# Optimization experiments

Measured on AMD Instinct MI355X. Metric: run time of the kernel, lower is better.

Reference implementation:

```python
import jax, jax.numpy as jnp
import numpy as np

# Production-scale dims (see shape_source)
T, H, W, C = 2, 384, 384, 128
HEADS, WIN = 4, 8
HD = C // HEADS            # head_dim = 32
SCALE = HD ** -0.5
N = WIN * WIN              # tokens per window = 64
DN = ('NCHW', 'OIHW', 'NCHW')


def setup_inputs() -> dict:
    key = jax.random.key(0)
    ks = jax.random.split(key, 16)
    p = lambda k, shp: jax.random.normal(k, shp, jnp.float32) * 0.02
    inp = {
        'vid': jax.random.normal(ks[0], (T, H, W, C), jnp.float32),
        'rpb_table': p(ks[1], ((2 * WIN - 1) * (2 * WIN - 1), HEADS)),
    }
    i = 2
    for nm in ('q', 'k', 'v'):  # SepConv2d: depthwise 3x3 + ReLU + pointwise 1x1
        inp[nm + '_dw'] = p(ks[i], (C, 1, 3, 3)); i += 1
        inp[nm + '_dwb'] = p(ks[i], (C,)); i += 1
        inp[nm + '_pw'] = p(ks[i], (C, C, 1, 1)); i += 1
        inp[nm + '_pwb'] = p(ks[i], (C,)); i += 1
    inp['proj_w'] = p(ks[14], (C, C))
    inp['proj_b'] = p(ks[15], (C,))
    return inp


def _sepconv(x, dw, dwb, pw, pwb):
    # x: [T, C, H, W]; Uformer SepConv2d = depthwise 3x3 -> ReLU -> pointwise 1x1
    y = jax.lax.conv_general_dilated(x, dw, (1, 1), 'SAME',
                                     feature_group_count=C, dimension_numbers=DN)
    y = jax.nn.relu(y + dwb[None, :, None, None])
    y = jax.lax.conv_general_dilated(y, pw, (1, 1), 'SAME', dimension_numbers=DN)
    return y + pwb[None, :, None, None]


def _to_windows(x):
    # [T, C, H, W] -> [T*nWh*nWw, heads, N, hd]
    x = x.reshape(T, HEADS, HD, H // WIN, WIN, W // WIN, WIN)
    x = x.transpose(0, 3, 5, 1, 4, 6, 2)
    return x.reshape(-1, HEADS, N, HD)


def _rel_bias(rpb_table):
    # Swin-style relative position index for an 8x8 window
    r = jnp.arange(WIN)
    coords = jnp.stack(jnp.meshgrid(r, r, indexing='ij')).reshape(2, -1)  # [2, N]
    rel = coords[:, :, None] - coords[:, None, :]                          # [2, N, N]
    idx = (rel[0] + WIN - 1) * (2 * WIN - 1) + (rel[1] + WIN - 1)          # [N, N]
    return rpb_table[idx].transpose(2, 0, 1)                               # [heads, N, N]


def reference(vid, rpb_table,
              q_dw, q_dwb, q_pw, q_pwb,
              k_dw, k_dwb, k_pw, k_pwb,
              v_dw, v_dwb, v_pw, v_pwb,
              proj_w, proj_b):
    x = vid.transpose(0, 3, 1, 2)                      # t h w c -> t c h w
    q = _sepconv(x, q_dw, q_dwb, q_pw, q_pwb) * SCALE  # q scaled as in forward
    k = _sepconv(x, k_dw, k_dwb, k_pw, k_pwb)
    v = _sepconv(x, v_dw, v_dwb, v_pw, v_pwb)
    qw, kw, vw = _to_windows(q), _to_windows(k), _to_windows(v)
    # rel-pos-biased softmax attention within each 8x8 window (ws==8 branch)
    attn = jnp.einsum('whnd,whmd->whnm', qw, kw) + _rel_bias(rpb_table)[None]
    attn = jax.nn.softmax(attn, axis=-1)
    out = jnp.einsum('whnm,whmd->whnd', attn, vw)      # weighted patch sum (ps=1)
    out = out.transpose(0, 2, 1, 3).reshape(-1, N, C)  # merge heads -> [nW, N, C]
    out = out @ proj_w.T + proj_b                      # nn.Linear(dim, dim)
    # windows back to video; iFoldz with ps=1, stride0=1 => zvid==1 (identity norm)
    Hn, Wn = H // WIN, W // WIN
    out = out.reshape(T, Hn, Wn, WIN, WIN, C).transpose(0, 1, 3, 2, 4, 5)
    return out.reshape(T, H, W, C)
```

## Files before the change

kernel.cpp:

```cpp
#include <hip/hip_runtime.h>
#include <hip/hip_fp16.h>
#include <stdint.h>

#define T_ 2
#define H_ 384
#define W_ 384
#define C_ 128
#define HN_ 48
#define WN_ 48
#define NWIN_ (T_*HN_*WN_)
#define SCALE_ 0.17677669529663687f

typedef float f32x4 __attribute__((ext_vector_type(4)));
typedef _Float16 f16x8 __attribute__((ext_vector_type(8)));

#define WS_WFRAG 0
#define WS_BIASX 131072
#define WS_DWF   196608
#define WS_DWB   205824

#define TMP_OFF 0
#define KB_OFF  16384
#define VB_OFF  32768
#define WL_OFF  49152
#define SMEM_SZ 81920

#define GLOBAL_AS __attribute__((address_space(1)))
#define LDS_AS    __attribute__((address_space(3)))

__device__ __forceinline__ void g2l16(const void* g, void* l){
  __builtin_amdgcn_global_load_lds((const GLOBAL_AS unsigned int*)g,
                                   (LDS_AS unsigned int*)l, 16, 0, 0);
}

__device__ __forceinline__ unsigned int pkh(float a, float b){
  union{__half2 h; unsigned int u;} c;
  c.h = __float22half2_rn(make_float2(a, b));
  return c.u;
}
__device__ __forceinline__ unsigned short f2h(float f){
  union{__half h; unsigned short u;} c; c.h = __float2half_rn(f); return c.u;
}
__device__ __forceinline__ __half2 u2h(unsigned int u){
  union{unsigned int u; __half2 h;} c; c.u = u; return c.h;
}
__device__ __forceinline__ unsigned int relu2u(__half2 v){
  union{__half2 h; unsigned int u;} c; c.h = v;
  const unsigned int m = ((c.u >> 15) & 0x00010001u) * 0xFFFFu;
  return c.u & ~m;
}
__device__ __forceinline__ int swz256(int row, int b){ return row*256 + (b ^ ((row & 15) << 4)); }
__device__ __forceinline__ int swz128(int row, int b){ return row*128 + (b ^ ((row & 7) << 4)); }

__device__ __forceinline__ f16x8 xpose_frag(uint2 a, uint2 b, int l0b, int l1b, int hi){
  union{ f16x8 v; unsigned int u[4]; } r;
  const unsigned x0 = __builtin_amdgcn_ds_bpermute(l0b, (int)a.x);
  const unsigned y0 = __builtin_amdgcn_ds_bpermute(l0b, (int)b.x);
  const unsigned x1 = __builtin_amdgcn_ds_bpermute(l0b, (int)a.y);
  const unsigned y1 = __builtin_amdgcn_ds_bpermute(l0b, (int)b.y);
  const unsigned x2 = __builtin_amdgcn_ds_bpermute(l1b, (int)a.x);
  const unsigned y2 = __builtin_amdgcn_ds_bpermute(l1b, (int)b.x);
  const unsigned x3 = __builtin_amdgcn_ds_bpermute(l1b, (int)a.y);
  const unsigned y3 = __builtin_amdgcn_ds_bpermute(l1b, (int)b.y);
  r.u[0] = hi ? y0 : x0; r.u[1] = hi ? y1 : x1;
  r.u[2] = hi ? y2 : x2; r.u[3] = hi ? y3 : x3;
  return r.v;
}

__global__ __launch_bounds__(256)
void prep_kernel(const float* __restrict__ qpw, const float* __restrict__ kpw,
                 const float* __restrict__ vpw, const float* __restrict__ pjw,
                 const float* __restrict__ rpb,
                 const float* __restrict__ qdw, const float* __restrict__ kdw,
                 const float* __restrict__ vdw,
                 const float* __restrict__ qdwb, const float* __restrict__ kdwb,
                 const float* __restrict__ vdwb,
                 ushort* __restrict__ wfrag, float* __restrict__ biasx,
                 unsigned int* __restrict__ dwf, unsigned int* __restrict__ dwb2)
{
  const int idx = blockIdx.x*256 + threadIdx.x;
  if (idx < 8192) {
    const int mat = idx >> 11, rem = idx & 2047;
    const int nt8 = rem >> 8, ks = (rem >> 6) & 3, lane = rem & 63;
    const int c16 = lane & 15, g = lane >> 4;
    const float* Ws[4] = {qpw, kpw, vpw, pjw};
    const float* src = Ws[mat] + (nt8*16 + c16)*128 + ks*32 + g*8;
    ushort* dst = wfrag + idx*8;
    #pragma unroll
    for (int e = 0; e < 8; ++e) dst[e] = f2h(src[e]);
  } else if (idx < 24576) {
    const int i2 = idx - 8192;
    const int he = i2 >> 12;
    const int m2 = (i2 >> 10) & 3;
    const int n  = (i2 >> 4) & 63;
    const int gr = i2 & 15;
    const int m  = m2*16 + gr;
    const int ny = n >> 3, nx = n & 7, my = m >> 3, mx = m & 7;
    biasx[i2] = rpb[((ny - my + 7)*15 + (nx - mx + 7))*4 + he];
  } else if (idx < 24576 + 2304) {
    const int i2 = idx - 24576;
    const int p = i2 / 768, rem = i2 % 768, cp = rem / 12, j = rem % 12;
    const float* dws[3] = {qdw, kdw, vdw};
    unsigned int v = 0;
    if (j < 9) v = pkh(dws[p][(2*cp)*9 + j], dws[p][(2*cp+1)*9 + j]);
    dwf[(p*64 + cp)*12 + j] = v;
  } else if (idx < 24576 + 2304 + 192) {
    const int i2 = idx - 24576 - 2304;
    const int p = i2 >> 6, cp = i2 & 63;
    const float* dbs[3] = {qdwb, kdwb, vdwb};
    dwb2[p*64 + cp] = pkh(dbs[p][2*cp], dbs[p][2*cp+1]);
  }
}

__global__ __launch_bounds__(512, 8)
void winattn_v4(const float* __restrict__ vid,
                const float* __restrict__ qpwb, const float* __restrict__ kpwb,
                const float* __restrict__ vpwb, const float* __restrict__ pjb,
                const ushort* __restrict__ wfrag, const float* __restrict__ biasx,
                const unsigned int* __restrict__ dwf, const unsigned int* __restrict__ dwb2,
                float* __restrict__ out)
{
  __shared__ __attribute__((aligned(16))) char smem[SMEM_SZ];
  char* tmpb = smem + TMP_OFF;
  char* kb   = smem + KB_OFF;
  char* vb   = smem + VB_OFF;
  char* wl   = smem + WL_OFF;

  const int tid  = threadIdx.x;
  const int w    = tid >> 6;
  const int lane = tid & 63;
  const int g    = lane >> 4;
  const int c16  = lane & 15;
  const int hi   = (lane >= 32);
  const int l0b  = (((g & 1) << 5) + c16) << 2;
  const int l1b  = l0b + 64;

  auto stage_w = [&](int m){
    const char* gsrc = reinterpret_cast<const char*>(wfrag) + m*32768;
    #pragma unroll
    for (int i2 = 0; i2 < 4; ++i2){
      const int off = (i2*512 + tid)*16;
      g2l16(gsrc + off, wl + off);
    }
  };

  const int wid = (blockIdx.x & 7) * (NWIN_ / 8) + (blockIdx.x >> 3);
  const int t  = wid / (HN_*WN_);
  const int hw = wid % (HN_*WN_);
  const int hn = hw / WN_, wn = hw % WN_;
  const int h0 = hn*8, w0 = wn*8;

  const int mt  = w & 3;
  const int ntb = (w >> 2) * 4;
  const int n0  = mt*16 + g*4;
  const int he = w >> 1, half = w & 1;
  const int y = w;

  stage_w(1);

  __half2 hx[3][10];
  #pragma unroll
  for (int dy = 0; dy < 3; ++dy){
    const int hh = h0 + y - 1 + dy;
    const bool rv = (unsigned)hh < (unsigned)H_;
    #pragma unroll
    for (int xc = 0; xc < 10; ++xc){
      const int ww = w0 - 1 + xc;
      float2 l = make_float2(0.f, 0.f);
      if (rv && (unsigned)ww < (unsigned)W_)
        l = *reinterpret_cast<const float2*>(&vid[(((long)t*H_ + hh)*W_ + ww)*C_ + 2*lane]);
      hx[dy][xc] = __float22half2_rn(l);
    }
  }

  auto dw_pass = [&](int p){
    const uint4* dq = reinterpret_cast<const uint4*>(dwf + (p*64 + lane)*12);
    const uint4 wA = dq[0], wB = dq[1], wC = dq[2];
    const __half2 w9[9] = { u2h(wA.x), u2h(wA.y), u2h(wA.z), u2h(wA.w),
                            u2h(wB.x), u2h(wB.y), u2h(wB.z), u2h(wB.w), u2h(wC.x) };
    const __half2 b2 = u2h(dwb2[p*64 + lane]);
    __half2 acc[8];
    #pragma unroll
    for (int px = 0; px < 8; ++px) acc[px] = b2;
    #pragma unroll
    for (int dy = 0; dy < 3; ++dy)
      #pragma unroll
      for (int dx = 0; dx < 3; ++dx){
        const __half2 w2 = w9[dy*3+dx];
        #pragma unroll
        for (int px = 0; px < 8; ++px)
          acc[px] = __hfma2(hx[dy][px+dx], w2, acc[px]);
      }
    #pragma unroll
    for (int px = 0; px < 8; ++px)
      *reinterpret_cast<unsigned int*>(tmpb + swz256(y*8+px, 4*lane)) = relu2u(acc[px]);
  };

  dw_pass(1);
  __syncthreads();
  {
    #pragma unroll
    for (int nh = 0; nh < 2; ++nh){
      f32x4 a2[2] = {{0.f,0.f,0.f,0.f},{0.f,0.f,0.f,0.f}};
      #pragma unroll
      for (int ks = 0; ks < 4; ++ks){
        const f16x8 af = *reinterpret_cast<const f16x8*>(tmpb + swz256(mt*16+c16, ks*64 + g*16));
        #pragma unroll
        for (int j = 0; j < 2; ++j){
          const f16x8 bf = *reinterpret_cast<const f16x8*>(wl + (((ntb+nh*2+j)*4 + ks)*64 + lane)*16);
          a2[j] = __builtin_amdgcn_mfma_f32_16x16x32_f16(af, bf, a2[j], 0, 0, 0);
        }
      }
      #pragma unroll
      for (int j = 0; j < 2; ++j){
        const int co = (ntb+nh*2+j)*16 + c16;
        const float bias = kpwb[co];
        const unsigned int u01 = pkh(a2[j][0]+bias, a2[j][1]+bias);
        const unsigned int u23 = pkh(a2[j][2]+bias, a2[j][3]+bias);
        *reinterpret_cast<ushort*>(kb + swz256(n0+0, 2*co)) = (ushort)u01;
        *reinterpret_cast<ushort*>(kb + swz256(n0+1, 2*co)) = (ushort)(u01 >> 16);
        *reinterpret_cast<ushort*>(kb + swz256(n0+2, 2*co)) = (ushort)u23;
        *reinterpret_cast<ushort*>(kb + swz256(n0+3, 2*co)) = (ushort)(u23 >> 16);
      }
    }
  }
  __syncthreads();

  stage_w(2);
  dw_pass(2);
  __syncthreads();
  {
    #pragma unroll
    for (int nh = 0; nh < 2; ++nh){
      f32x4 a2[2] = {{0.f,0.f,0.f,0.f},{0.f,0.f,0.f,0.f}};
      #pragma unroll
      for (int ks = 0; ks < 4; ++ks){
        const f16x8 af = *reinterpret_cast<const f16x8*>(tmpb + swz256(mt*16+c16, ks*64 + g*16));
        #pragma unroll
        for (int j = 0; j < 2; ++j){
          const f16x8 bf = *reinterpret_cast<const f16x8*>(wl + (((ntb+nh*2+j)*4 + ks)*64 + lane)*16);
          a2[j] = __builtin_amdgcn_mfma_f32_16x16x32_f16(af, bf, a2[j], 0, 0, 0);
        }
      }
      #pragma unroll
      for (int j = 0; j < 2; ++j){
        const int co = (ntb+nh*2+j)*16 + c16;
        const float bias = vpwb[co];
        const uint2 pk2 = make_uint2(pkh(a2[j][0]+bias, a2[j][1]+bias),
                                     pkh(a2[j][2]+bias, a2[j][3]+bias));
        *reinterpret_cast<uint2*>(vb + swz128(co, 2*n0)) = pk2;
      }
    }
  }
  __syncthreads();

  stage_w(0);
  dw_pass(0);
  __syncthreads();
  f16x8 qfrag[2];
  {
    uint2 pkq[2][2];
    #pragma unroll
    for (int dt = 0; dt < 2; ++dt){
      f32x4 aq[2] = {{0.f,0.f,0.f,0.f},{0.f,0.f,0.f,0.f}};
      #pragma unroll
      for (int ks = 0; ks < 4; ++ks){
        const f16x8 awf = *reinterpret_cast<const f16x8*>(wl + (((he*2+dt)*4 + ks)*64 + lane)*16);
        #pragma unroll
        for (int qt = 0; qt < 2; ++qt){
          const f16x8 btf = *reinterpret_cast<const f16x8*>(tmpb + swz256(half*32+qt*16+c16, ks*64 + g*16));
          aq[qt] = __builtin_amdgcn_mfma_f32_16x16x32_f16(awf, btf, aq[qt], 0, 0, 0);
        }
      }
      const float4 qb4 = *reinterpret_cast<const float4*>(&qpwb[he*32 + dt*16 + g*4]);
      #pragma unroll
      for (int qt = 0; qt < 2; ++qt){
        pkq[dt][qt] = make_uint2(pkh((aq[qt][0]+qb4.x)*SCALE_, (aq[qt][1]+qb4.y)*SCALE_),
                                 pkh((aq[qt][2]+qb4.z)*SCALE_, (aq[qt][3]+qb4.w)*SCALE_));
      }
    }
    #pragma unroll
    for (int qt = 0; qt < 2; ++qt)
      qfrag[qt] = xpose_frag(pkq[0][qt], pkq[1][qt], l0b, l1b, hi);
  }
  __syncthreads();

  stage_w(3);
  f16x8 pf[2][2];
  #pragma unroll
  for (int qt = 0; qt < 2; ++qt){
    f32x4 st[4];
    #pragma unroll
    for (int m2 = 0; m2 < 4; ++m2){
      const f16x8 kf = *reinterpret_cast<const f16x8*>(kb + swz256(m2*16 + c16, he*64 + g*16));
      const f32x4 z = {0.f,0.f,0.f,0.f};
      st[m2] = __builtin_amdgcn_mfma_f32_16x16x32_f16(kf, qfrag[qt], z, 0, 0, 0);
    }
    const int n = half*32 + qt*16 + c16;
    float mx = -1e30f;
    #pragma unroll
    for (int m2 = 0; m2 < 4; ++m2){
      const float4 bx = *reinterpret_cast<const float4*>(&biasx[(((he*4+m2)*64 + n) << 4) + (g << 2)]);
      st[m2][0] += bx.x; st[m2][1] += bx.y; st[m2][2] += bx.z; st[m2][3] += bx.w;
      mx = fmaxf(mx, fmaxf(fmaxf(st[m2][0], st[m2][1]), fmaxf(st[m2][2], st[m2][3])));
    }
    mx = fmaxf(mx, __shfl_xor(mx, 16));
    mx = fmaxf(mx, __shfl_xor(mx, 32));
    float ls = 0.f;
    #pragma unroll
    for (int m2 = 0; m2 < 4; ++m2){
      #pragma unroll
      for (int r = 0; r < 4; ++r){
        st[m2][r] = __expf(st[m2][r] - mx);
        ls += st[m2][r];
      }
    }
    ls += __shfl_xor(ls, 16);
    ls += __shfl_xor(ls, 32);
    const float inv = 1.0f / ls;
    uint2 pk[4];
    #pragma unroll
    for (int m2 = 0; m2 < 4; ++m2)
      pk[m2] = make_uint2(pkh(st[m2][0]*inv, st[m2][1]*inv),
                          pkh(st[m2][2]*inv, st[m2][3]*inv));
    #pragma unroll
    for (int ks = 0; ks < 2; ++ks)
      pf[qt][ks] = xpose_frag(pk[2*ks], pk[2*ks+1], l0b, l1b, hi);
  }
  {
    f32x4 o[2][2];
    #pragma unroll
    for (int qt = 0; qt < 2; ++qt)
      #pragma unroll
      for (int dt = 0; dt < 2; ++dt) o[qt][dt] = (f32x4){0.f,0.f,0.f,0.f};
    #pragma unroll
    for (int ks = 0; ks < 2; ++ks){
      #pragma unroll
      for (int dt = 0; dt < 2; ++dt){
        const f16x8 vf = *reinterpret_cast<const f16x8*>(vb + swz128(he*32+dt*16+c16, ks*64 + g*16));
        #pragma unroll
        for (int qt = 0; qt < 2; ++qt)
          o[qt][dt] = __builtin_amdgcn_mfma_f32_16x16x32_f16(pf[qt][ks], vf, o[qt][dt], 0, 0, 0);
      }
    }
    #pragma unroll
    for (int qt = 0; qt < 2; ++qt)
      #pragma unroll
      for (int dt = 0; dt < 2; ++dt){
        const int d2 = he*32 + dt*16 + c16;
        const int nb = half*32 + qt*16 + g*4;
        const unsigned int u01 = pkh(o[qt][dt][0], o[qt][dt][1]);
        const unsigned int u23 = pkh(o[qt][dt][2], o[qt][dt][3]);
        *reinterpret_cast<ushort*>(tmpb + swz256(nb+0, 2*d2)) = (ushort)u01;
        *reinterpret_cast<ushort*>(tmpb + swz256(nb+1, 2*d2)) = (ushort)(u01 >> 16);
        *reinterpret_cast<ushort*>(tmpb + swz256(nb+2, 2*d2)) = (ushort)u23;
        *reinterpret_cast<ushort*>(tmpb + swz256(nb+3, 2*d2)) = (ushort)(u23 >> 16);
      }
  }
  __syncthreads();

  {
    #pragma unroll
    for (int nh = 0; nh < 2; ++nh){
      f32x4 a2[2] = {{0.f,0.f,0.f,0.f},{0.f,0.f,0.f,0.f}};
      #pragma unroll
      for (int ks = 0; ks < 4; ++ks){
        const f16x8 af = *reinterpret_cast<const f16x8*>(tmpb + swz256(mt*16+c16, ks*64 + g*16));
        #pragma unroll
        for (int j = 0; j < 2; ++j){
          const f16x8 bf = *reinterpret_cast<const f16x8*>(wl + (((ntb+nh*2+j)*4 + ks)*64 + lane)*16);
          a2[j] = __builtin_amdgcn_mfma_f32_16x16x32_f16(af, bf, a2[j], 0, 0, 0);
        }
      }
      #pragma unroll
      for (int j = 0; j < 2; ++j){
        const int co = (ntb+nh*2+j)*16 + c16;
        const float bias = pjb[co];
        #pragma unroll
        for (int r = 0; r < 4; ++r){
          const int n = n0 + r;
          out[(((long)t*H_ + (h0+(n>>3)))*W_ + (w0+(n&7)))*C_ + co] = a2[j][r] + bias;
        }
      }
    }
  }
}

extern "C" void kernel_launch(void* const* d_in, const int* in_sizes, int n_in,
                              void* d_out, int out_size, void* d_ws, size_t ws_size,
                              hipStream_t stream) {
  const float* vid  = (const float*)d_in[0];
  const float* rpb  = (const float*)d_in[1];
  const float* qdw  = (const float*)d_in[2];
  const float* qdwb = (const float*)d_in[3];
  const float* qpw  = (const float*)d_in[4];
  const float* qpwb = (const float*)d_in[5];
  const float* kdw  = (const float*)d_in[6];
  const float* kdwb = (const float*)d_in[7];
  const float* kpw  = (const float*)d_in[8];
  const float* kpwb = (const float*)d_in[9];
  const float* vdw  = (const float*)d_in[10];
  const float* vdwb = (const float*)d_in[11];
  const float* vpw  = (const float*)d_in[12];
  const float* vpwb = (const float*)d_in[13];
  const float* pjw  = (const float*)d_in[14];
  const float* pjb  = (const float*)d_in[15];
  float* outp = (float*)d_out;

  ushort*       wfrag = (ushort*)((char*)d_ws + WS_WFRAG);
  float*        biasx = (float*)((char*)d_ws + WS_BIASX);
  unsigned int* dwf   = (unsigned int*)((char*)d_ws + WS_DWF);
  unsigned int* dwb2  = (unsigned int*)((char*)d_ws + WS_DWB);

  prep_kernel<<<dim3(106), dim3(256), 0, stream>>>(
      qpw, kpw, vpw, pjw, rpb, qdw, kdw, vdw, qdwb, kdwb, vdwb,
      wfrag, biasx, dwf, dwb2);
  winattn_v4<<<dim3(NWIN_), dim3(512), 0, stream>>>(
      vid, qpwb, kpwb, vpwb, pjb, wfrag, biasx, dwf, dwb2, outp);
}
```

Measured before the change: 164.7 us.

## Run all three depthwise passes up front and reorder Q/K/V stages

All three depthwise 3x3 passes now run back to back from the same register-held input tile, writing into three separate shared buffers. This removes two barrier-separated depthwise phases. Q is projected first, reading its pointwise weights straight from global workspace rather than a staged LDS copy. The softmax scores are computed before the V projection, and LDS buffer roles are rotated to match. This trims barriers and stage_w round-trips, at the cost of uncached global weight reads for Q and longer live ranges that may raise register pressure.

```diff
diff --git a/kernel.cpp b/kernel.cpp
--- a/kernel.cpp
+++ b/kernel.cpp
@@ -113,7 +113,7 @@
 }
 
 __global__ __launch_bounds__(512, 8)
-void winattn_v4(const float* __restrict__ vid,
+void winattn_v5(const float* __restrict__ vid,
                 const float* __restrict__ qpwb, const float* __restrict__ kpwb,
                 const float* __restrict__ vpwb, const float* __restrict__ pjb,
                 const ushort* __restrict__ wfrag, const float* __restrict__ biasx,
@@ -158,46 +158,77 @@
 
   stage_w(1);
 
-  __half2 hx[3][10];
-  #pragma unroll
-  for (int dy = 0; dy < 3; ++dy){
-    const int hh = h0 + y - 1 + dy;
-    const bool rv = (unsigned)hh < (unsigned)H_;
-    #pragma unroll
-    for (int xc = 0; xc < 10; ++xc){
-      const int ww = w0 - 1 + xc;
-      float2 l = make_float2(0.f, 0.f);
-      if (rv && (unsigned)ww < (unsigned)W_)
-        l = *reinterpret_cast<const float2*>(&vid[(((long)t*H_ + hh)*W_ + ww)*C_ + 2*lane]);
-      hx[dy][xc] = __float22half2_rn(l);
-    }
-  }
-
-  auto dw_pass = [&](int p){
-    const uint4* dq = reinterpret_cast<const uint4*>(dwf + (p*64 + lane)*12);
-    const uint4 wA = dq[0], wB = dq[1], wC = dq[2];
-    const __half2 w9[9] = { u2h(wA.x), u2h(wA.y), u2h(wA.z), u2h(wA.w),
-                            u2h(wB.x), u2h(wB.y), u2h(wB.z), u2h(wB.w), u2h(wC.x) };
-    const __half2 b2 = u2h(dwb2[p*64 + lane]);
-    __half2 acc[8];
-    #pragma unroll
-    for (int px = 0; px < 8; ++px) acc[px] = b2;
-    #pragma unroll
-    for (int dy = 0; dy < 3; ++dy)
-      #pragma unroll
-      for (int dx = 0; dx < 3; ++dx){
-        const __half2 w2 = w9[dy*3+dx];
-        #pragma unroll
-        for (int px = 0; px < 8; ++px)
-          acc[px] = __hfma2(hx[dy][px+dx], w2, acc[px]);
-      }
-    #pragma unroll
-    for (int px = 0; px < 8; ++px)
-      *reinterpret_cast<unsigned int*>(tmpb + swz256(y*8+px, 4*lane)) = relu2u(acc[px]);
-  };
-
-  dw_pass(1);
-  __syncthreads();
+  {
+    __half2 hx[3][10];
+    #pragma unroll
+    for (int dy = 0; dy < 3; ++dy){
+      const int hh = h0 + y - 1 + dy;
+      const bool rv = (unsigned)hh < (unsigned)H_;
+      #pragma unroll
+      for (int xc = 0; xc < 10; ++xc){
+        const int ww = w0 - 1 + xc;
+        float2 l = make_float2(0.f, 0.f);
+        if (rv && (unsigned)ww < (unsigned)W_)
+          l = *reinterpret_cast<const float2*>(&vid[(((long)t*H_ + hh)*W_ + ww)*C_ + 2*lane]);
+        hx[dy][xc] = __float22half2_rn(l);
+      }
+    }
+    auto dw_pass = [&](int p, char* dst){
+      const uint4* dq = reinterpret_cast<const uint4*>(dwf + (p*64 + lane)*12);
+      const uint4 wA = dq[0], wB = dq[1], wC = dq[2];
+      const __half2 w9[9] = { u2h(wA.x), u2h(wA.y), u2h(wA.z), u2h(wA.w),
+                              u2h(wB.x), u2h(wB.y), u2h(wB.z), u2h(wB.w), u2h(wC.x) };
+      const __half2 b2 = u2h(dwb2[p*64 + lane]);
+      __half2 acc[8];
+      #pragma unroll
+      for (int px = 0; px < 8; ++px) acc[px] = b2;
+      #pragma unroll
+      for (int dy = 0; dy < 3; ++dy)
+        #pragma unroll
+        for (int dx = 0; dx < 3; ++dx){
+          const __half2 w2 = w9[dy*3+dx];
+          #pragma unroll
+          for (int px = 0; px < 8; ++px)
+            acc[px] = __hfma2(hx[dy][px+dx], w2, acc[px]);
+        }
+      #pragma unroll
+      for (int px = 0; px < 8; ++px)
+        *reinterpret_cast<unsigned int*>(dst + swz256(y*8+px, 4*lane)) = relu2u(acc[px]);
+    };
+    dw_pass(1, tmpb);
+    dw_pass(2, vb);
+    dw_pass(0, kb);
+  }
+  __syncthreads();
+
+  f16x8 qfrag[2];
+  {
+    uint2 pkq[2][2];
+    #pragma unroll
+    for (int dt = 0; dt < 2; ++dt){
+      f32x4 aq[2] = {{0.f,0.f,0.f,0.f},{0.f,0.f,0.f,0.f}};
+      #pragma unroll
+      for (int ks = 0; ks < 4; ++ks){
+        const f16x8 awf = *reinterpret_cast<const f16x8*>(&wfrag[(((he*2+dt)*4 + ks)*64 + lane)*8]);
+        #pragma unroll
+        for (int qt = 0; qt < 2; ++qt){
+          const f16x8 btf = *reinterpret_cast<const f16x8*>(kb + swz256(half*32+qt*16+c16, ks*64 + g*16));
+          aq[qt] = __builtin_amdgcn_mfma_f32_16x16x32_f16(awf, btf, aq[qt], 0, 0, 0);
+        }
+      }
+      const float4 qb4 = *reinterpret_cast<const float4*>(&qpwb[he*32 + dt*16 + g*4]);
+      #pragma unroll
+      for (int qt = 0; qt < 2; ++qt){
+        pkq[dt][qt] = make_uint2(pkh((aq[qt][0]+qb4.x)*SCALE_, (aq[qt][1]+qb4.y)*SCALE_),
+                                 pkh((aq[qt][2]+qb4.z)*SCALE_, (aq[qt][3]+qb4.w)*SCALE_));
+      }
+    }
+    #pragma unroll
+    for (int qt = 0; qt < 2; ++qt)
+      qfrag[qt] = xpose_frag(pkq[0][qt], pkq[1][qt], l0b, l1b, hi);
+  }
+  __syncthreads();
+
   {
     #pragma unroll
     for (int nh = 0; nh < 2; ++nh){
@@ -227,15 +258,56 @@
   __syncthreads();
 
   stage_w(2);
-  dw_pass(2);
-  __syncthreads();
+  f16x8 pf[2][2];
+  #pragma unroll
+  for (int qt = 0; qt < 2; ++qt){
+    f32x4 st[4];
+    #pragma unroll
+    for (int m2 = 0; m2 < 4; ++m2){
+      const f16x8 kf = *reinterpret_cast<const f16x8*>(kb + swz256(m2*16 + c16, he*64 + g*16));
+      const f32x4 z = {0.f,0.f,0.f,0.f};
+      st[m2] = __builtin_amdgcn_mfma_f32_16x16x32_f16(kf, qfrag[qt], z, 0, 0, 0);
+    }
+    const int n = half*32 + qt*16 + c16;
+    float mx = -1e30f;
+    #pragma unroll
+    for (int m2 = 0; m2 < 4; ++m2){
+      const float4 bx = *reinterpret_cast<const float4*>(&biasx[(((he*4+m2)*64 + n) << 4) + (g << 2)]);
+      st[m2][0] += bx.x; st[m2][1] += bx.y; st[m2][2] += bx.z; st[m2][3] += bx.w;
+      mx = fmaxf(mx, fmaxf(fmaxf(st[m2][0], st[m2][1]), fmaxf(st[m2][2], st[m2][3])));
+    }
+    mx = fmaxf(mx, __shfl_xor(mx, 16));
+    mx = fmaxf(mx, __shfl_xor(mx, 32));
+    float ls = 0.f;
+    #pragma unroll
+    for (int m2 = 0; m2 < 4; ++m2){
+      #pragma unroll
+      for (int r = 0; r < 4; ++r){
+        st[m2][r] = __expf(st[m2][r] - mx);
+        ls += st[m2][r];
+      }
+    }
+    ls += __shfl_xor(ls, 16);
+    ls += __shfl_xor(ls, 32);
+    const float inv = 1.0f / ls;
+    uint2 pk[4];
+    #pragma unroll
+    for (int m2 = 0; m2 < 4; ++m2)
+      pk[m2] = make_uint2(pkh(st[m2][0]*inv, st[m2][1]*inv),
+                          pkh(st[m2][2]*inv, st[m2][3]*inv));
+    #pragma unroll
+    for (int ks = 0; ks < 2; ++ks)
+      pf[qt][ks] = xpose_frag(pk[2*ks], pk[2*ks+1], l0b, l1b, hi);
+  }
+  __syncthreads();
+
   {
     #pragma unroll
     for (int nh = 0; nh < 2; ++nh){
       f32x4 a2[2] = {{0.f,0.f,0.f,0.f},{0.f,0.f,0.f,0.f}};
       #pragma unroll
       for (int ks = 0; ks < 4; ++ks){
-        const f16x8 af = *reinterpret_cast<const f16x8*>(tmpb + swz256(mt*16+c16, ks*64 + g*16));
+        const f16x8 af = *reinterpret_cast<const f16x8*>(vb + swz256(mt*16+c16, ks*64 + g*16));
         #pragma unroll
         for (int j = 0; j < 2; ++j){
           const f16x8 bf = *reinterpret_cast<const f16x8*>(wl + (((ntb+nh*2+j)*4 + ks)*64 + lane)*16);
@@ -248,96 +320,24 @@
         const float bias = vpwb[co];
         const uint2 pk2 = make_uint2(pkh(a2[j][0]+bias, a2[j][1]+bias),
                                      pkh(a2[j][2]+bias, a2[j][3]+bias));
-        *reinterpret_cast<uint2*>(vb + swz128(co, 2*n0)) = pk2;
-      }
-    }
-  }
-  __syncthreads();
-
-  stage_w(0);
-  dw_pass(0);
-  __syncthreads();
-  f16x8 qfrag[2];
-  {
-    uint2 pkq[2][2];
-    #pragma unroll
-    for (int dt = 0; dt < 2; ++dt){
-      f32x4 aq[2] = {{0.f,0.f,0.f,0.f},{0.f,0.f,0.f,0.f}};
-      #pragma unroll
-      for (int ks = 0; ks < 4; ++ks){
-        const f16x8 awf = *reinterpret_cast<const f16x8*>(wl + (((he*2+dt)*4 + ks)*64 + lane)*16);
-        #pragma unroll
-        for (int qt = 0; qt < 2; ++qt){
-          const f16x8 btf = *reinterpret_cast<const f16x8*>(tmpb + swz256(half*32+qt*16+c16, ks*64 + g*16));
-          aq[qt] = __builtin_amdgcn_mfma_f32_16x16x32_f16(awf, btf, aq[qt], 0, 0, 0);
-        }
-      }
-      const float4 qb4 = *reinterpret_cast<const float4*>(&qpwb[he*32 + dt*16 + g*4]);
-      #pragma unroll
-      for (int qt = 0; qt < 2; ++qt){
-        pkq[dt][qt] = make_uint2(pkh((aq[qt][0]+qb4.x)*SCALE_, (aq[qt][1]+qb4.y)*SCALE_),
-                                 pkh((aq[qt][2]+qb4.z)*SCALE_, (aq[qt][3]+qb4.w)*SCALE_));
-      }
-    }
+        *reinterpret_cast<uint2*>(tmpb + swz128(co, 2*n0)) = pk2;
+      }
+    }
+  }
+  __syncthreads();
+
+  stage_w(3);
+  {
+    f32x4 o[2][2];
     #pragma unroll
     for (int qt = 0; qt < 2; ++qt)
-      qfrag[qt] = xpose_frag(pkq[0][qt], pkq[1][qt], l0b, l1b, hi);
-  }
-  __syncthreads();
-
-  stage_w(3);
-  f16x8 pf[2][2];
-  #pragma unroll
-  for (int qt = 0; qt < 2; ++qt){
-    f32x4 st[4];
-    #pragma unroll
-    for (int m2 = 0; m2 < 4; ++m2){
-      const f16x8 kf = *reinterpret_cast<const f16x8*>(kb + swz256(m2*16 + c16, he*64 + g*16));
-      const f32x4 z = {0.f,0.f,0.f,0.f};
-      st[m2] = __builtin_amdgcn_mfma_f32_16x16x32_f16(kf, qfrag[qt], z, 0, 0, 0);
-    }
-    const int n = half*32 + qt*16 + c16;
-    float mx = -1e30f;
-    #pragma unroll
-    for (int m2 = 0; m2 < 4; ++m2){
-      const float4 bx = *reinterpret_cast<const float4*>(&biasx[(((he*4+m2)*64 + n) << 4) + (g << 2)]);
-      st[m2][0] += bx.x; st[m2][1] += bx.y; st[m2][2] += bx.z; st[m2][3] += bx.w;
-      mx = fmaxf(mx, fmaxf(fmaxf(st[m2][0], st[m2][1]), fmaxf(st[m2][2], st[m2][3])));
-    }
-    mx = fmaxf(mx, __shfl_xor(mx, 16));
-    mx = fmaxf(mx, __shfl_xor(mx, 32));
-    float ls = 0.f;
-    #pragma unroll
-    for (int m2 = 0; m2 < 4; ++m2){
-      #pragma unroll
-      for (int r = 0; r < 4; ++r){
-        st[m2][r] = __expf(st[m2][r] - mx);
-        ls += st[m2][r];
-      }
-    }
-    ls += __shfl_xor(ls, 16);
-    ls += __shfl_xor(ls, 32);
-    const float inv = 1.0f / ls;
-    uint2 pk[4];
-    #pragma unroll
-    for (int m2 = 0; m2 < 4; ++m2)
-      pk[m2] = make_uint2(pkh(st[m2][0]*inv, st[m2][1]*inv),
-                          pkh(st[m2][2]*inv, st[m2][3]*inv));
-    #pragma unroll
-    for (int ks = 0; ks < 2; ++ks)
-      pf[qt][ks] = xpose_frag(pk[2*ks], pk[2*ks+1], l0b, l1b, hi);
-  }
-  {
-    f32x4 o[2][2];
-    #pragma unroll
-    for (int qt = 0; qt < 2; ++qt)
       #pragma unroll
       for (int dt = 0; dt < 2; ++dt) o[qt][dt] = (f32x4){0.f,0.f,0.f,0.f};
     #pragma unroll
     for (int ks = 0; ks < 2; ++ks){
       #pragma unroll
       for (int dt = 0; dt < 2; ++dt){
-        const f16x8 vf = *reinterpret_cast<const f16x8*>(vb + swz128(he*32+dt*16+c16, ks*64 + g*16));
+        const f16x8 vf = *reinterpret_cast<const f16x8*>(tmpb + swz128(he*32+dt*16+c16, ks*64 + g*16));
         #pragma unroll
         for (int qt = 0; qt < 2; ++qt)
           o[qt][dt] = __builtin_amdgcn_mfma_f32_16x16x32_f16(pf[qt][ks], vf, o[qt][dt], 0, 0, 0);
@@ -351,10 +351,10 @@
         const int nb = half*32 + qt*16 + g*4;
         const unsigned int u01 = pkh(o[qt][dt][0], o[qt][dt][1]);
         const unsigned int u23 = pkh(o[qt][dt][2], o[qt][dt][3]);
-        *reinterpret_cast<ushort*>(tmpb + swz256(nb+0, 2*d2)) = (ushort)u01;
-        *reinterpret_cast<ushort*>(tmpb + swz256(nb+1, 2*d2)) = (ushort)(u01 >> 16);
-        *reinterpret_cast<ushort*>(tmpb + swz256(nb+2, 2*d2)) = (ushort)u23;
-        *reinterpret_cast<ushort*>(tmpb + swz256(nb+3, 2*d2)) = (ushort)(u23 >> 16);
+        *reinterpret_cast<ushort*>(vb + swz256(nb+0, 2*d2)) = (ushort)u01;
+        *reinterpret_cast<ushort*>(vb + swz256(nb+1, 2*d2)) = (ushort)(u01 >> 16);
+        *reinterpret_cast<ushort*>(vb + swz256(nb+2, 2*d2)) = (ushort)u23;
+        *reinterpret_cast<ushort*>(vb + swz256(nb+3, 2*d2)) = (ushort)(u23 >> 16);
       }
   }
   __syncthreads();
@@ -365,7 +365,7 @@
       f32x4 a2[2] = {{0.f,0.f,0.f,0.f},{0.f,0.f,0.f,0.f}};
       #pragma unroll
       for (int ks = 0; ks < 4; ++ks){
-        const f16x8 af = *reinterpret_cast<const f16x8*>(tmpb + swz256(mt*16+c16, ks*64 + g*16));
+        const f16x8 af = *reinterpret_cast<const f16x8*>(vb + swz256(mt*16+c16, ks*64 + g*16));
         #pragma unroll
         for (int j = 0; j < 2; ++j){
           const f16x8 bf = *reinterpret_cast<const f16x8*>(wl + (((ntb+nh*2+j)*4 + ks)*64 + lane)*16);
@@ -415,6 +415,6 @@
   prep_kernel<<<dim3(106), dim3(256), 0, stream>>>(
       qpw, kpw, vpw, pjw, rpb, qdw, kdw, vdw, qdwb, kdwb, vdwb,
       wfrag, biasx, dwf, dwb2);
-  winattn_v4<<<dim3(NWIN_), dim3(512), 0, stream>>>(
+  winattn_v5<<<dim3(NWIN_), dim3(512), 0, stream>>>(
       vid, qpwb, kpwb, vpwb, pjb, wfrag, biasx, dwf, dwb2, outp);
 }
```

Measured after the change: 162.9 us (median of 2 runs). No clear change (-1.1%).
